# Kernel tuning notes

Measured on AMD Instinct MI355X. Metric: run time of the kernel, lower is better.

Reference implementation:

```python
import jax, jax.numpy as jnp
import numpy as np

IN_CH = 512
SCALES = (128.0, 256.0, 512.0)
ASPECT_RATIOS = (0.5, 1.0, 2.0)
NUM_ANCHORS = 9
PRE_NMS_TOPK = 10000
POST_NMS_TOPK = 2000
NMS_THRESH = 0.7


def conv2d(x, w, b, pad):
    y = jax.lax.conv_general_dilated(
        x, w, window_strides=(1, 1), padding=[(pad, pad), (pad, pad)],
        dimension_numbers=('NCHW', 'OIHW', 'NCHW'))
    return y + b[None, :, None, None]


def generate_anchors(image_hw, feat_hw, dtype=jnp.float32):
    img_h, img_w = image_hw
    gh, gw = feat_hw
    stride_h = img_h // gh
    stride_w = img_w // gw
    scale = jnp.asarray(SCALES, dtype)
    ar = jnp.asarray(ASPECT_RATIOS, dtype)
    h_ratio = jnp.sqrt(ar)
    w_ratio = 1.0 / h_ratio
    ws = (w_ratio[:, None] * scale[None, :]).reshape(-1)  # (9,) ratio-major
    hs = (h_ratio[:, None] * scale[None, :]).reshape(-1)
    base = jnp.round(jnp.stack([-ws, -hs, ws, hs], axis=1) / 2.0)  # (9,4)
    shift_x = jnp.arange(gw, dtype=dtype) * stride_w
    shift_y = jnp.arange(gh, dtype=dtype) * stride_h
    sy, sx = jnp.meshgrid(shift_y, shift_x, indexing='ij')
    sx = sx.reshape(-1)
    sy = sy.reshape(-1)
    shifts = jnp.stack([sx, sy, sx, sy], axis=1)  # (gh*gw, 4)
    anchors = (shifts[:, None, :] + base[None, :, :]).reshape(-1, 4)
    return anchors


def decode_boxes(deltas, anchors):
    # deltas: (N,4) [dx,dy,dw,dh]; anchors: (N,4) [x1,y1,x2,y2]
    w = anchors[:, 2] - anchors[:, 0]
    h = anchors[:, 3] - anchors[:, 1]
    cx = anchors[:, 0] + 0.5 * w
    cy = anchors[:, 1] + 0.5 * h
    dx, dy, dw, dh = deltas[:, 0], deltas[:, 1], deltas[:, 2], deltas[:, 3]
    pcx = w * dx + cx
    pcy = h * dy + cy
    pw = jnp.exp(dw) * w
    ph = jnp.exp(dh) * h
    return jnp.stack([pcx - 0.5 * pw, pcy - 0.5 * ph,
                      pcx + 0.5 * pw, pcy + 0.5 * ph], axis=1)


def clamp_boxes(b, image_hw):
    h, w = image_hw
    return jnp.stack([jnp.clip(b[:, 0], 0.0, w), jnp.clip(b[:, 1], 0.0, h),
                      jnp.clip(b[:, 2], 0.0, w), jnp.clip(b[:, 3], 0.0, h)], axis=1)


def pairwise_iou(boxes1, boxes2):
    area1 = (boxes1[:, 2] - boxes1[:, 0]) * (boxes1[:, 3] - boxes1[:, 1])
    area2 = (boxes2[:, 2] - boxes2[:, 0]) * (boxes2[:, 3] - boxes2[:, 1])
    xl = jnp.maximum(boxes1[:, None, 0], boxes2[None, :, 0])
    yt = jnp.maximum(boxes1[:, None, 1], boxes2[None, :, 1])
    xr = jnp.minimum(boxes1[:, None, 2], boxes2[None, :, 2])
    yb = jnp.minimum(boxes1[:, None, 3], boxes2[None, :, 3])
    inter = jnp.clip(xr - xl, 0.0) * jnp.clip(yb - yt, 0.0)
    return inter / (area1[:, None] + area2[None, :] - inter)


def nms_keep(boxes_sorted, thresh):
    # boxes already sorted by score descending; returns bool keep mask
    n = boxes_sorted.shape[0]
    iou = pairwise_iou(boxes_sorted, boxes_sorted)  # (n,n) ~ the memory-bound hot spot
    idx = jnp.arange(n)
    def body(i, keep):
        suppressed = jnp.any((iou[i] > thresh) & keep & (idx < i))
        return keep.at[i].set(jnp.logical_not(suppressed))
    return jax.lax.fori_loop(0, n, body, jnp.ones((n,), dtype=bool))


def filter_proposals(proposals, logits, image_hw):
    scores = jax.nn.sigmoid(logits.reshape(-1))
    top_scores, top_idx = jax.lax.top_k(scores, PRE_NMS_TOPK)  # sorted descending
    props = proposals[top_idx]
    props = clamp_boxes(props, image_hw)
    keep = nms_keep(jax.lax.stop_gradient(props), NMS_THRESH)
    masked = jnp.where(keep, jax.lax.stop_gradient(top_scores), -1.0)
    sel_scores, sel = jax.lax.top_k(masked, POST_NMS_TOPK)
    valid = sel_scores >= 0.0  # sigmoid scores are >0; padded slots are -1
    out_boxes = jnp.where(valid[:, None], props[sel], 0.0)
    out_scores = jnp.where(valid, top_scores[sel], 0.0)
    return out_boxes, out_scores


def setup_inputs() -> dict:
    key = jax.random.key(0)
    ks = jax.random.split(key, 6)
    image = jax.random.normal(ks[0], (1, 3, 800, 800), jnp.float32)
    feat = jax.random.normal(ks[1], (1, IN_CH, 50, 50), jnp.float32)
    # small init scales keep exp(dw) numerically tame (mimics real conv init)
    rpn_w = jax.random.normal(ks[2], (IN_CH, IN_CH, 3, 3), jnp.float32) * 0.02
    rpn_b = jnp.zeros((IN_CH,), jnp.float32)
    cls_w = jax.random.normal(ks[3], (NUM_ANCHORS, IN_CH, 1, 1), jnp.float32) * 0.01
    cls_b = jnp.zeros((NUM_ANCHORS,), jnp.float32)
    box_w = jax.random.normal(ks[4], (NUM_ANCHORS * 4, IN_CH, 1, 1), jnp.float32) * 0.01
    box_b = jnp.zeros((NUM_ANCHORS * 4,), jnp.float32)
    return {"image": image, "feat": feat, "rpn_w": rpn_w, "rpn_b": rpn_b,
            "cls_w": cls_w, "cls_b": cls_b, "box_w": box_w, "box_b": box_b}


def reference(image, feat, rpn_w, rpn_b, cls_w, cls_b, box_w, box_b):
    B, _, H, W = feat.shape  # B == 1 as in the original (single-image RPN)
    rpn_feat = jax.nn.relu(conv2d(feat, rpn_w, rpn_b, pad=1))
    cls = conv2d(rpn_feat, cls_w, cls_b, pad=0)        # (1, 9, H, W)
    box = conv2d(rpn_feat, box_w, box_b, pad=0)        # (1, 36, H, W)
    anchors = generate_anchors(image.shape[-2:], (H, W), feat.dtype)  # (H*W*9, 4)
    # cls: NCHW -> NHWC -> (N_anchors, 1), anchor order = (y, x, anchor)
    cls_flat = jnp.transpose(cls, (0, 2, 3, 1)).reshape(-1, 1)
    # box: (1,9,4,H,W) -> (1,H,W,9,4) -> (N_anchors, 4)
    deltas = jnp.transpose(box.reshape(B, NUM_ANCHORS, 4, H, W), (0, 3, 4, 1, 2)).reshape(-1, 4)
    proposals = decode_boxes(deltas, anchors)
    props, scores = filter_proposals(proposals, jax.lax.stop_gradient(cls_flat), image.shape[-2:])
    return props, scores, cls_flat
```

## Files before the change

### kernel.cpp

```cpp
#include <hip/hip_runtime.h>
#include <cstdint>
#include <cstddef>


typedef unsigned long long ull;
typedef double d4 __attribute__((ext_vector_type(4)));

#define NANCH 9
#define NPIX  2500
#define CIN   512
#define COUT  512
#define KTOT  4608
#define KSEG  2304
#define NBOX  22500
#define TOPK1 10000
#define TOPK2 2000
#define WORDS 157
#define NHEAD 45
#define HPAD  48

__global__ __launch_bounds__(128, 2) void conv_gemm(const float* __restrict__ feat,
                                                    const float* __restrict__ w,
                                                    double* __restrict__ part) {
  const int p0  = blockIdx.x * 32;
  const int co0 = blockIdx.y * 64;
  const int z   = blockIdx.z;
  const int kseg0 = z * KSEG;
  __shared__ double As[2][16][36];
  __shared__ double Bs[2][16][68];
  const int tid  = threadIdx.x;
  const int lane = tid & 63;
  const int wave = tid >> 6;
  const int quad = lane >> 4;
  const int l16  = lane & 15;
  const int wp = wave * 16;
  const int plB = tid & 31;
  const int kB0 = tid >> 5;
  const int pB = p0 + plB;
  const int py = pB / 50, px = pB - py * 50;
  const int coA = tid >> 1;
  const int kA2 = (tid & 1) * 8;

  int pmap[4];
  {
    double av_p = (quad == 0) ? (double)(l16 + 1) : (quad == 1 ? 1.0 : 0.0);
    double bv_p = (quad == 0) ? 1.0 : (quad == 1 ? (double)(1000 * (l16 + 1)) : 0.0);
    d4 dp = (d4){0.0, 0.0, 0.0, 0.0};
    dp = __builtin_amdgcn_mfma_f64_16x16x4f64(av_p, bv_p, dp, 0, 0, 0);
#pragma unroll
    for (int r = 0; r < 4; ++r) {
      int iv = (int)(dp[r] + 0.5);
      int mm = iv % 1000 - 1;
      int nn = iv / 1000 - 1;
      pmap[r] = (mm & 255) | (nn << 8);
    }
  }

  d4 acc[4];
#pragma unroll
  for (int i = 0; i < 4; ++i) acc[i] = (d4){0.0, 0.0, 0.0, 0.0};

  const float* wbase = w + (size_t)(co0 + coA) * KTOT + kseg0 + kA2;
  const int NCH = KSEG / 16;

  {
    float4 wb0a = *(const float4*)(wbase);
    float4 wb0b = *(const float4*)(wbase + 4);
    float fb0[4];
#pragma unroll
    for (int jj = 0; jj < 4; ++jj) {
      int k = kseg0 + kB0 + 4 * jj;
      int ci = k / 9, r = k - ci * 9, ky = r / 3, kx = r - ky * 3;
      int yy = py + ky - 1, xx = px + kx - 1;
      float v = 0.0f;
      if (pB < NPIX && yy >= 0 && yy < 50 && xx >= 0 && xx < 50)
        v = feat[ci * NPIX + yy * 50 + xx];
      fb0[jj] = v;
    }
    Bs[0][kA2 + 0][coA] = (double)wb0a.x;
    Bs[0][kA2 + 1][coA] = (double)wb0a.y;
    Bs[0][kA2 + 2][coA] = (double)wb0a.z;
    Bs[0][kA2 + 3][coA] = (double)wb0a.w;
    Bs[0][kA2 + 4][coA] = (double)wb0b.x;
    Bs[0][kA2 + 5][coA] = (double)wb0b.y;
    Bs[0][kA2 + 6][coA] = (double)wb0b.z;
    Bs[0][kA2 + 7][coA] = (double)wb0b.w;
#pragma unroll
    for (int jj = 0; jj < 4; ++jj) As[0][kB0 + 4 * jj][plB] = (double)fb0[jj];
  }
  float4 wb1a = *(const float4*)(wbase + 16);
  float4 wb1b = *(const float4*)(wbase + 20);
  float fb1[4];
#pragma unroll
  for (int jj = 0; jj < 4; ++jj) {
    int k = kseg0 + 16 + kB0 + 4 * jj;
    int ci = k / 9, r = k - ci * 9, ky = r / 3, kx = r - ky * 3;
    int yy = py + ky - 1, xx = px + kx - 1;
    float v = 0.0f;
    if (pB < NPIX && yy >= 0 && yy < 50 && xx >= 0 && xx < 50)
      v = feat[ci * NPIX + yy * 50 + xx];
    fb1[jj] = v;
  }
  __syncthreads();

  for (int c = 0; c < NCH; ++c) {
    const int buf = c & 1;
    if (c + 1 < NCH) {
      Bs[buf ^ 1][kA2 + 0][coA] = (double)wb1a.x;
      Bs[buf ^ 1][kA2 + 1][coA] = (double)wb1a.y;
      Bs[buf ^ 1][kA2 + 2][coA] = (double)wb1a.z;
      Bs[buf ^ 1][kA2 + 3][coA] = (double)wb1a.w;
      Bs[buf ^ 1][kA2 + 4][coA] = (double)wb1b.x;
      Bs[buf ^ 1][kA2 + 5][coA] = (double)wb1b.y;
      Bs[buf ^ 1][kA2 + 6][coA] = (double)wb1b.z;
      Bs[buf ^ 1][kA2 + 7][coA] = (double)wb1b.w;
#pragma unroll
      for (int jj = 0; jj < 4; ++jj)
        As[buf ^ 1][kB0 + 4 * jj][plB] = (double)fb1[jj];
    }
    if (c + 2 < NCH) {
      wb1a = *(const float4*)(wbase + (c + 2) * 16);
      wb1b = *(const float4*)(wbase + (c + 2) * 16 + 4);
#pragma unroll
      for (int jj = 0; jj < 4; ++jj) {
        int k = kseg0 + (c + 2) * 16 + kB0 + 4 * jj;
        int ci = k / 9, r = k - ci * 9, ky = r / 3, kx = r - ky * 3;
        int yy = py + ky - 1, xx = px + kx - 1;
        float v = 0.0f;
        if (pB < NPIX && yy >= 0 && yy < 50 && xx >= 0 && xx < 50)
          v = feat[ci * NPIX + yy * 50 + xx];
        fb1[jj] = v;
      }
    }
#pragma unroll
    for (int kk = 0; kk < 16; kk += 4) {
      double av  = As[buf][kk + quad][wp + l16];
      double bv0 = Bs[buf][kk + quad][ 0 + l16];
      double bv1 = Bs[buf][kk + quad][16 + l16];
      double bv2 = Bs[buf][kk + quad][32 + l16];
      double bv3 = Bs[buf][kk + quad][48 + l16];
      acc[0] = __builtin_amdgcn_mfma_f64_16x16x4f64(av, bv0, acc[0], 0, 0, 0);
      acc[1] = __builtin_amdgcn_mfma_f64_16x16x4f64(av, bv1, acc[1], 0, 0, 0);
      acc[2] = __builtin_amdgcn_mfma_f64_16x16x4f64(av, bv2, acc[2], 0, 0, 0);
      acc[3] = __builtin_amdgcn_mfma_f64_16x16x4f64(av, bv3, acc[3], 0, 0, 0);
    }
    __syncthreads();
  }
  double* basez = part + (size_t)z * COUT * NPIX;
#pragma unroll
  for (int cj = 0; cj < 4; ++cj) {
#pragma unroll
    for (int r = 0; r < 4; ++r) {
      int mm = pmap[r] & 255, nn = pmap[r] >> 8;
      int p  = p0 + wp + mm;
      int co = co0 + cj * 16 + nn;
      if (p < NPIX) basez[(size_t)co * NPIX + p] = acc[cj][r];
    }
  }
}

__global__ __launch_bounds__(256) void heads_mm(
    const double* __restrict__ part, const float* __restrict__ rpn_b,
    const float* __restrict__ cls_w, const float* __restrict__ box_w,
    double* __restrict__ headsc) {
  const int lane = threadIdx.x & 63;
  const int o = __builtin_amdgcn_readfirstlane(blockIdx.y * 4 + (threadIdx.x >> 6));
  if (o >= NHEAD) return;
  const int p = blockIdx.x * 64 + lane;
  const bool act = p < NPIX;
  const int pp = act ? p : 0;
  const float* wsel = (o < 9) ? (cls_w + (size_t)o * CIN)
                              : (box_w + (size_t)(o - 9) * CIN);
  const double* p0 = part + pp;
  const double* p1 = part + (size_t)COUT * NPIX + pp;
  double acc = 0.0;
#pragma unroll 4
  for (int co = 0; co < CIN; ++co) {
    double v = p0[(size_t)co * NPIX] + p1[(size_t)co * NPIX] + (double)rpn_b[co];
    v = v > 0.0 ? v : 0.0;
    acc += (double)wsel[co] * v;
  }
  if (act) headsc[(size_t)p * HPAD + o] = acc;
}

__global__ __launch_bounds__(256) void decode_kernel(
    const double* __restrict__ headsc, const float* __restrict__ cls_b,
    const float* __restrict__ box_b, double* __restrict__ logits,
    double* __restrict__ boxesAll, float* __restrict__ out_cls) {
  int idx = blockIdx.x * blockDim.x + threadIdx.x;
  if (idx >= NBOX) return;
  int p = idx / 9, a = idx - p * 9;
  int y = p / 50, x = p - y * 50;
  double sx = 16.0 * (double)x, sy = 16.0 * (double)y;
  const double scs[3] = {128.0, 256.0, 512.0};
  const double ars[3] = {0.5, 1.0, 2.0};
  double ar = ars[a / 3], sc = scs[a - (a / 3) * 3];
  double hr = sqrt(ar), wr = 1.0 / hr;
  double wv = wr * sc, hv = hr * sc;
  double bx0 = rint(-wv * 0.5), by0 = rint(-hv * 0.5);
  double bx1 = rint(wv * 0.5), by1 = rint(hv * 0.5);
  double a0 = sx + bx0, a1 = sy + by0, a2 = sx + bx1, a3 = sy + by1;
  double wA = a2 - a0, hA = a3 - a1;
  double cx = a0 + 0.5 * wA, cy = a1 + 0.5 * hA;
  const double* hp = headsc + (size_t)p * HPAD;
  double dx = hp[9 + a * 4 + 0] + (double)box_b[a * 4 + 0];
  double dy = hp[9 + a * 4 + 1] + (double)box_b[a * 4 + 1];
  double dw = hp[9 + a * 4 + 2] + (double)box_b[a * 4 + 2];
  double dh = hp[9 + a * 4 + 3] + (double)box_b[a * 4 + 3];
  double pcx = wA * dx + cx, pcy = hA * dy + cy;
  double pw = exp(dw) * wA, ph = exp(dh) * hA;
  double b0 = pcx - 0.5 * pw, b1 = pcy - 0.5 * ph;
  double b2 = pcx + 0.5 * pw, b3 = pcy + 0.5 * ph;
  b0 = fmin(fmax(b0, 0.0), 800.0);
  b1 = fmin(fmax(b1, 0.0), 800.0);
  b2 = fmin(fmax(b2, 0.0), 800.0);
  b3 = fmin(fmax(b3, 0.0), 800.0);
  boxesAll[(size_t)idx * 4 + 0] = b0;
  boxesAll[(size_t)idx * 4 + 1] = b1;
  boxesAll[(size_t)idx * 4 + 2] = b2;
  boxesAll[(size_t)idx * 4 + 3] = b3;
  double L = hp[a] + (double)cls_b[a];
  logits[idx] = L;
  out_cls[idx] = (float)L;
}

__global__ __launch_bounds__(256) void rank_count(const double* __restrict__ logits,
                                                  int* __restrict__ ranks) {
  __shared__ double Ls[2048];
  int i = blockIdx.x * 256 + threadIdx.x;
  int j0 = blockIdx.y * 2048;
  int jn = NBOX - j0;
  if (jn > 2048) jn = 2048;
  for (int t = threadIdx.x; t < jn; t += 256) Ls[t] = logits[j0 + t];
  __syncthreads();
  if (i >= NBOX) return;
  double Li = logits[i];
  int cnt = 0;
  for (int t = 0; t < jn; ++t) {
    double Lj = Ls[t];
    int j = j0 + t;
    cnt += (Lj > Li || (Lj == Li && j < i)) ? 1 : 0;
  }
  atomicAdd(&ranks[i], cnt);
}

__global__ __launch_bounds__(256) void scatter_topk(const double* __restrict__ logits,
                                                    const double* __restrict__ boxesAll,
                                                    const int* __restrict__ ranks,
                                                    double* __restrict__ sLog,
                                                    double* __restrict__ sBox) {
  int i = blockIdx.x * 256 + threadIdx.x;
  if (i >= NBOX) return;
  int r = ranks[i];
  if (r < TOPK1) {
    sLog[r] = logits[i];
    sBox[(size_t)r * 4 + 0] = boxesAll[(size_t)i * 4 + 0];
    sBox[(size_t)r * 4 + 1] = boxesAll[(size_t)i * 4 + 1];
    sBox[(size_t)r * 4 + 2] = boxesAll[(size_t)i * 4 + 2];
    sBox[(size_t)r * 4 + 3] = boxesAll[(size_t)i * 4 + 3];
  }
}

__global__ __launch_bounds__(256) void iou_mask(const double* __restrict__ sb,
                                                ull* __restrict__ mask) {
  const int it = blockIdx.x;
  const int wt = blockIdx.y;
  if (wt * 4 + 3 < it) return;
  __shared__ double ib[64][4];
  __shared__ double jb[256][4];
  const int tid = threadIdx.x;
  {
    int ii = it * 64 + (tid >> 2);
    int d = tid & 3;
    ib[tid >> 2][d] = (ii < TOPK1) ? sb[(size_t)ii * 4 + d] : 0.0;
  }
  for (int t = tid; t < 1024; t += 256) {
    int jj = wt * 256 + (t >> 2);
    jb[t >> 2][t & 3] = (jj < TOPK1) ? sb[(size_t)jj * 4 + (t & 3)] : 0.0;
  }
  __syncthreads();
  const int il = tid & 63, wl = tid >> 6;
  const int i = it * 64 + il;
  const int word = wt * 4 + wl;
  if (i >= TOPK1 || word >= WORDS || word < (i >> 6)) return;
  const double x0 = ib[il][0], y0 = ib[il][1], x1 = ib[il][2], y1 = ib[il][3];
  const double areai = (x1 - x0) * (y1 - y0);
  ull bits = 0;
  const int jbase = word * 64;
  for (int b = 0; b < 64; ++b) {
    int j = jbase + b;
    if (j <= i || j >= TOPK1) continue;
    int jl = wl * 64 + b;
    double u0 = jb[jl][0], u1 = jb[jl][1], u2 = jb[jl][2], u3 = jb[jl][3];
    double xl = fmax(x0, u0), yt = fmax(y0, u1);
    double xr = fmin(x1, u2), yb = fmin(y1, u3);
    double iw = xr - xl, ih = yb - yt;
    iw = iw > 0.0 ? iw : 0.0;
    ih = ih > 0.0 ? ih : 0.0;
    double inter = iw * ih;
    double aj = (u2 - u0) * (u3 - u1);
    double un = areai + aj - inter;
    if (inter > 0.7 * un) bits |= 1ull << b;
  }
  mask[(size_t)i * WORDS + word] = bits;
}

#define NTILE 8
#define TRS   10
#define KCAP  2112

__global__ __launch_bounds__(256) void nms_scan(const ull* __restrict__ mask,
                                                ull* __restrict__ keepwords) {
  __shared__ ull tileRows[512 * TRS];
  __shared__ int klist[KCAP];
  __shared__ ull remvPart[32][NTILE + 1];
  __shared__ unsigned int remv32[NTILE * 2];
  __shared__ int newk[64];
  __shared__ int kcLds, nkLds, doneLds;
  const int tid = threadIdx.x;
  const int lane = tid & 63;
  const int wave = tid >> 6;
  if (tid == 0) { kcLds = 0; nkLds = 0; doneLds = 0; }
  __syncthreads();

  for (int T = 0; T < (WORDS + NTILE - 1) / NTILE; ++T) {
    const int G0 = T * NTILE;
    const int TW = (WORDS - G0 < NTILE) ? (WORDS - G0) : NTILE;
    const int kc0 = kcLds;
#pragma unroll
    for (int pass = 0; pass < 8; ++pass) {
      int lr = pass * 64 + (tid >> 2);
      int w  = (tid & 3) * 2;
      int gr = G0 * 64 + lr;
      ull v0 = 0, v1 = 0;
      if (gr < TOPK1) {
        const ull* row = mask + (size_t)gr * WORDS + G0;
        if (w < TW)     v0 = row[w];
        if (w + 1 < TW) v1 = row[w + 1];
      }
      tileRows[lr * TRS + w]     = v0;
      tileRows[lr * TRS + w + 1] = v1;
    }
    {
      int w = tid & 7, stripe = tid >> 3;
      ull acc = 0;
      if (w < TW) {
        int t = stripe;
        for (; t + 224 < kc0; t += 256) {
          ull a0 = mask[(size_t)klist[t      ] * WORDS + G0 + w];
          ull a1 = mask[(size_t)klist[t +  32] * WORDS + G0 + w];
          ull a2 = mask[(size_t)klist[t +  64] * WORDS + G0 + w];
          ull a3 = mask[(size_t)klist[t +  96] * WORDS + G0 + w];
          ull a4 = mask[(size_t)klist[t + 128] * WORDS + G0 + w];
          ull a5 = mask[(size_t)klist[t + 160] * WORDS + G0 + w];
          ull a6 = mask[(size_t)klist[t + 192] * WORDS + G0 + w];
          ull a7 = mask[(size_t)klist[t + 224] * WORDS + G0 + w];
          acc |= ((a0 | a1) | (a2 | a3)) | ((a4 | a5) | (a6 | a7));
        }
        for (; t < kc0; t += 32) acc |= mask[(size_t)klist[t] * WORDS + G0 + w];
      }
      remvPart[stripe][w] = acc;
    }
    __syncthreads();
    if (tid < NTILE) {
      ull r = 0;
#pragma unroll
      for (int s = 0; s < 32; ++s) r |= remvPart[s][tid];
      remv32[tid * 2]     = (unsigned int)r;
      remv32[tid * 2 + 1] = (unsigned int)(r >> 32);
    }
    __syncthreads();
    for (int gi = 0; gi < TW; ++gi) {
      const int g = G0 + gi;
      if (wave == 0) {
        ull cur = ((ull)remv32[gi * 2 + 1] << 32) | remv32[gi * 2];
        unsigned int clo = __builtin_amdgcn_readfirstlane((unsigned int)cur);
        unsigned int chi = __builtin_amdgcn_readfirstlane((unsigned int)(cur >> 32));
        cur = ((ull)chi << 32) | clo;
        ull mrow = tileRows[(gi * 64 + lane) * TRS + gi];
        const unsigned int ml = (unsigned int)mrow;
        const unsigned int mh = (unsigned int)(mrow >> 32);
        const ull validm = (g == WORDS - 1) ? 0xFFFFull : ~0ull;
        ull rem = (~cur) & validm;
        while (rem) {
          int b = __ffsll((long long)rem) - 1;
          b = __builtin_amdgcn_readfirstlane(b);
          ull m = ((ull)(unsigned int)__builtin_amdgcn_readlane((int)mh, b) << 32) |
                  (unsigned int)__builtin_amdgcn_readlane((int)ml, b);
          cur |= m;
          ull above = (b == 63) ? 0ull : (~0ull << (b + 1));
          rem = (~cur) & rem & above;
        }
        ull kb = (~cur) & validm;
        if (lane == 0) keepwords[g] = kb;
        int kc = kcLds;
        if ((kb >> lane) & 1ull) {
          int ofs = __popcll(lane ? (kb & ((1ull << lane) - 1ull)) : 0ull);
          klist[kc + ofs] = g * 64 + lane;
          newk[ofs] = gi * 64 + lane;
        }
        if (lane == 0) {
          int nk = __popcll(kb);
          nkLds = nk;
          kcLds = kc + nk;
          doneLds = (kc + nk >= TOPK2) ? 1 : 0;
        }
      }
      __syncthreads();
      if (doneLds) break;
      if (gi + 1 < TW) {
        int w = tid & 7, k0 = tid >> 3;
        int nk = nkLds;
        if (w > gi && w < TW) {
          ull acc = 0;
          for (int kk = k0; kk < nk; kk += 32) acc |= tileRows[newk[kk] * TRS + w];
          if (acc) {
            atomicOr(&remv32[w * 2], (unsigned int)acc);
            atomicOr(&remv32[w * 2 + 1], (unsigned int)(acc >> 32));
          }
        }
      }
      __syncthreads();
    }
    if (doneLds) break;
  }
}

__global__ __launch_bounds__(256) void finalize_kernel(const ull* __restrict__ keepwords,
                                                       const double* __restrict__ sBox,
                                                       const double* __restrict__ sLog,
                                                       float* __restrict__ out) {
  __shared__ int pref[WORDS];
  int t = threadIdx.x;
  if (t == 0) {
    int s = 0;
    for (int w = 0; w < WORDS; ++w) {
      pref[w] = s;
      s += __popcll(keepwords[w]);
    }
  }
  __syncthreads();
  if (t < WORDS) {
    ull kb = keepwords[t];
    int base = pref[t];
    while (kb) {
      int b = __ffsll((long long)kb) - 1;
      kb &= kb - 1;
      if (base < TOPK2) {
        int i = t * 64 + b;
        out[base * 4 + 0] = (float)sBox[(size_t)i * 4 + 0];
        out[base * 4 + 1] = (float)sBox[(size_t)i * 4 + 1];
        out[base * 4 + 2] = (float)sBox[(size_t)i * 4 + 2];
        out[base * 4 + 3] = (float)sBox[(size_t)i * 4 + 3];
        double L = sLog[i];
        out[TOPK2 * 4 + base] = (float)(1.0 / (1.0 + exp(-L)));
      }
      ++base;
    }
  }
}

extern "C" void kernel_launch(void* const* d_in, const int* in_sizes, int n_in,
                              void* d_out, int out_size, void* d_ws, size_t ws_size,
                              hipStream_t stream) {
  const float* feat  = (const float*)d_in[1];
  const float* rpn_w = (const float*)d_in[2];
  const float* rpn_b = (const float*)d_in[3];
  const float* cls_w = (const float*)d_in[4];
  const float* cls_b = (const float*)d_in[5];
  const float* box_w = (const float*)d_in[6];
  const float* box_b = (const float*)d_in[7];
  float* out = (float*)d_out;

  char* ws = (char*)d_ws;
  double* part     = (double*)(ws);
  double* logits   = (double*)(ws + 20480000);
  double* boxesAll = (double*)(ws + 20660000);
  int*    ranks    = (int*)   (ws + 21380000);
  double* sBox     = (double*)(ws + 21470000);
  double* sLog     = (double*)(ws + 21790000);
  ull*    mask     = (ull*)   (ws + 21870000);
  ull*    keepw    = (ull*)   (ws + 34430000);
  double* headsc   = (double*)(ws + 21870000);

  hipMemsetAsync(d_out, 0, (TOPK2 * 4 + TOPK2) * sizeof(float), stream);
  hipMemsetAsync(ranks, 0, NBOX * sizeof(int), stream);
  hipMemsetAsync(keepw, 0, WORDS * sizeof(ull), stream);

  conv_gemm<<<dim3(80, 8, 2), 128, 0, stream>>>(feat, rpn_w, part);
  heads_mm<<<dim3(40, 12), 256, 0, stream>>>(part, rpn_b, cls_w, box_w, headsc);
  decode_kernel<<<88, 256, 0, stream>>>(headsc, cls_b, box_b, logits, boxesAll,
                                        out + TOPK2 * 5);
  rank_count<<<dim3(88, 11), 256, 0, stream>>>(logits, ranks);
  scatter_topk<<<88, 256, 0, stream>>>(logits, boxesAll, ranks, sLog, sBox);
  iou_mask<<<dim3(WORDS, 40), 256, 0, stream>>>(sBox, mask);
  nms_scan<<<1, 256, 0, stream>>>(mask, keepw);
  finalize_kernel<<<1, 256, 0, stream>>>(keepw, sBox, sLog, out);
}
```

Baseline: 879.1 us.

## Store conv tiles as float in LDS and double the K-chunk per stage

Measured after the change: 873.1 us. About the same (-0.7%).

```diff
diff --git a/kernel.cpp b/kernel.cpp
--- a/kernel.cpp
+++ b/kernel.cpp
@@ -19,15 +19,15 @@
 #define NHEAD 45
 #define HPAD  48
 
-__global__ __launch_bounds__(128, 2) void conv_gemm(const float* __restrict__ feat,
+__global__ __launch_bounds__(128, 3) void conv_gemm(const float* __restrict__ feat,
                                                     const float* __restrict__ w,
                                                     double* __restrict__ part) {
   const int p0  = blockIdx.x * 32;
   const int co0 = blockIdx.y * 64;
   const int z   = blockIdx.z;
   const int kseg0 = z * KSEG;
-  __shared__ double As[2][16][36];
-  __shared__ double Bs[2][16][68];
+  __shared__ float As[2][32][40];
+  __shared__ float Bs[2][32][72];
   const int tid  = threadIdx.x;
   const int lane = tid & 63;
   const int wave = tid >> 6;
@@ -39,7 +39,7 @@
   const int pB = p0 + plB;
   const int py = pB / 50, px = pB - py * 50;
   const int coA = tid >> 1;
-  const int kA2 = (tid & 1) * 8;
+  const int kA2 = (tid & 1) * 16;
 
   int pmap[4];
   {
@@ -61,39 +61,40 @@
   for (int i = 0; i < 4; ++i) acc[i] = (d4){0.0, 0.0, 0.0, 0.0};
 
   const float* wbase = w + (size_t)(co0 + coA) * KTOT + kseg0 + kA2;
-  const int NCH = KSEG / 16;
+  const int NCH = KSEG / 32;
 
   {
-    float4 wb0a = *(const float4*)(wbase);
-    float4 wb0b = *(const float4*)(wbase + 4);
-    float fb0[4];
-#pragma unroll
-    for (int jj = 0; jj < 4; ++jj) {
+    float4 w0[4];
+#pragma unroll
+    for (int q = 0; q < 4; ++q) w0[q] = *(const float4*)(wbase + 4 * q);
+    float f0[8];
+#pragma unroll
+    for (int jj = 0; jj < 8; ++jj) {
       int k = kseg0 + kB0 + 4 * jj;
       int ci = k / 9, r = k - ci * 9, ky = r / 3, kx = r - ky * 3;
       int yy = py + ky - 1, xx = px + kx - 1;
       float v = 0.0f;
       if (pB < NPIX && yy >= 0 && yy < 50 && xx >= 0 && xx < 50)
         v = feat[ci * NPIX + yy * 50 + xx];
-      fb0[jj] = v;
-    }
-    Bs[0][kA2 + 0][coA] = (double)wb0a.x;
-    Bs[0][kA2 + 1][coA] = (double)wb0a.y;
-    Bs[0][kA2 + 2][coA] = (double)wb0a.z;
-    Bs[0][kA2 + 3][coA] = (double)wb0a.w;
-    Bs[0][kA2 + 4][coA] = (double)wb0b.x;
-    Bs[0][kA2 + 5][coA] = (double)wb0b.y;
-    Bs[0][kA2 + 6][coA] = (double)wb0b.z;
-    Bs[0][kA2 + 7][coA] = (double)wb0b.w;
-#pragma unroll
-    for (int jj = 0; jj < 4; ++jj) As[0][kB0 + 4 * jj][plB] = (double)fb0[jj];
-  }
-  float4 wb1a = *(const float4*)(wbase + 16);
-  float4 wb1b = *(const float4*)(wbase + 20);
-  float fb1[4];
-#pragma unroll
-  for (int jj = 0; jj < 4; ++jj) {
-    int k = kseg0 + 16 + kB0 + 4 * jj;
+      f0[jj] = v;
+    }
+#pragma unroll
+    for (int q = 0; q < 4; ++q) {
+      Bs[0][kA2 + 4 * q + 0][coA] = w0[q].x;
+      Bs[0][kA2 + 4 * q + 1][coA] = w0[q].y;
+      Bs[0][kA2 + 4 * q + 2][coA] = w0[q].z;
+      Bs[0][kA2 + 4 * q + 3][coA] = w0[q].w;
+    }
+#pragma unroll
+    for (int jj = 0; jj < 8; ++jj) As[0][kB0 + 4 * jj][plB] = f0[jj];
+  }
+  float4 wb1[4];
+#pragma unroll
+  for (int q = 0; q < 4; ++q) wb1[q] = *(const float4*)(wbase + 32 + 4 * q);
+  float fb1[8];
+#pragma unroll
+  for (int jj = 0; jj < 8; ++jj) {
+    int k = kseg0 + 32 + kB0 + 4 * jj;
     int ci = k / 9, r = k - ci * 9, ky = r / 3, kx = r - ky * 3;
     int yy = py + ky - 1, xx = px + kx - 1;
     float v = 0.0f;
@@ -106,24 +107,24 @@
   for (int c = 0; c < NCH; ++c) {
     const int buf = c & 1;
     if (c + 1 < NCH) {
-      Bs[buf ^ 1][kA2 + 0][coA] = (double)wb1a.x;
-      Bs[buf ^ 1][kA2 + 1][coA] = (double)wb1a.y;
-      Bs[buf ^ 1][kA2 + 2][coA] = (double)wb1a.z;
-      Bs[buf ^ 1][kA2 + 3][coA] = (double)wb1a.w;
-      Bs[buf ^ 1][kA2 + 4][coA] = (double)wb1b.x;
-      Bs[buf ^ 1][kA2 + 5][coA] = (double)wb1b.y;
-      Bs[buf ^ 1][kA2 + 6][coA] = (double)wb1b.z;
-      Bs[buf ^ 1][kA2 + 7][coA] = (double)wb1b.w;
-#pragma unroll
-      for (int jj = 0; jj < 4; ++jj)
-        As[buf ^ 1][kB0 + 4 * jj][plB] = (double)fb1[jj];
+#pragma unroll
+      for (int q = 0; q < 4; ++q) {
+        Bs[buf ^ 1][kA2 + 4 * q + 0][coA] = wb1[q].x;
+        Bs[buf ^ 1][kA2 + 4 * q + 1][coA] = wb1[q].y;
+        Bs[buf ^ 1][kA2 + 4 * q + 2][coA] = wb1[q].z;
+        Bs[buf ^ 1][kA2 + 4 * q + 3][coA] = wb1[q].w;
+      }
+#pragma unroll
+      for (int jj = 0; jj < 8; ++jj)
+        As[buf ^ 1][kB0 + 4 * jj][plB] = fb1[jj];
     }
     if (c + 2 < NCH) {
-      wb1a = *(const float4*)(wbase + (c + 2) * 16);
-      wb1b = *(const float4*)(wbase + (c + 2) * 16 + 4);
-#pragma unroll
-      for (int jj = 0; jj < 4; ++jj) {
-        int k = kseg0 + (c + 2) * 16 + kB0 + 4 * jj;
+#pragma unroll
+      for (int q = 0; q < 4; ++q)
+        wb1[q] = *(const float4*)(wbase + (c + 2) * 32 + 4 * q);
+#pragma unroll
+      for (int jj = 0; jj < 8; ++jj) {
+        int k = kseg0 + (c + 2) * 32 + kB0 + 4 * jj;
         int ci = k / 9, r = k - ci * 9, ky = r / 3, kx = r - ky * 3;
         int yy = py + ky - 1, xx = px + kx - 1;
         float v = 0.0f;
@@ -133,12 +134,12 @@
       }
     }
 #pragma unroll
-    for (int kk = 0; kk < 16; kk += 4) {
-      double av  = As[buf][kk + quad][wp + l16];
-      double bv0 = Bs[buf][kk + quad][ 0 + l16];
-      double bv1 = Bs[buf][kk + quad][16 + l16];
-      double bv2 = Bs[buf][kk + quad][32 + l16];
-      double bv3 = Bs[buf][kk + quad][48 + l16];
+    for (int kk = 0; kk < 32; kk += 4) {
+      double av  = (double)As[buf][kk + quad][wp + l16];
+      double bv0 = (double)Bs[buf][kk + quad][ 0 + l16];
+      double bv1 = (double)Bs[buf][kk + quad][16 + l16];
+      double bv2 = (double)Bs[buf][kk + quad][32 + l16];
+      double bv3 = (double)Bs[buf][kk + quad][48 + l16];
       acc[0] = __builtin_amdgcn_mfma_f64_16x16x4f64(av, bv0, acc[0], 0, 0, 0);
       acc[1] = __builtin_amdgcn_mfma_f64_16x16x4f64(av, bv1, acc[1], 0, 0, 0);
       acc[2] = __builtin_amdgcn_mfma_f64_16x16x4f64(av, bv2, acc[2], 0, 0, 0);
```
